# Performance work log

Measured on AMD Instinct MI355X. Metric: run time of the kernel, lower is better.

## Reference

```python
import jax, jax.numpy as jnp
import numpy as np

NEG_SLOPE = 0.2  # PyG GATv2Conv default negative_slope


def _gatv2(x, src, dst, Wl, Wr, att, bias, N, H, C):
    # GATv2: e_ij = att . leaky_relu(Wl x_j + Wr x_i); segment softmax over dst; scatter-add messages Wl x_j
    xl = (x @ Wl).reshape(N, H, C)  # source-side transform
    xr = (x @ Wr).reshape(N, H, C)  # target-side transform
    g = jax.nn.leaky_relu(xl[src] + xr[dst], NEG_SLOPE)  # [E, H, C]
    e = jnp.einsum('ehc,hc->eh', g, att)                 # [E, H]
    emax = jax.lax.stop_gradient(jax.ops.segment_max(e, dst, num_segments=N))
    p = jnp.exp(e - emax[dst])
    denom = jax.ops.segment_sum(p, dst, num_segments=N)
    alpha = p / denom[dst]                                # segment softmax [E, H]
    out = jax.ops.segment_sum(alpha[:, :, None] * xl[src], dst, num_segments=N)
    return out.reshape(N, H * C) + bias


def setup_inputs() -> dict:
    key = jax.random.key(0)
    N, E, F, H, C, L = 100000, 1000000, 128, 8, 10, 3
    ks = jax.random.split(key, 2 + 4 * L)
    inp = {
        'x': jax.random.normal(ks[0], (N, F), dtype=jnp.float32),
        'edge_index': jax.random.randint(ks[1], (2, E), 0, N, dtype=jnp.int32),
    }
    dims = [F] + [H * C] * (L - 1)
    for l in range(L):
        din = dims[l]
        s = 1.0 / np.sqrt(din)
        inp[f'Wl{l}'] = (jax.random.normal(ks[2 + 4 * l], (din, H * C)) * s).astype(jnp.float32)
        inp[f'Wr{l}'] = (jax.random.normal(ks[3 + 4 * l], (din, H * C)) * s).astype(jnp.float32)
        inp[f'att{l}'] = (jax.random.normal(ks[4 + 4 * l], (H, C)) * (1.0 / np.sqrt(C))).astype(jnp.float32)
        inp[f'b{l}'] = jnp.zeros((H * C,), jnp.float32)
    return inp


def reference(x, edge_index, Wl0, Wr0, att0, b0, Wl1, Wr1, att1, b1, Wl2, Wr2, att2, b2):
    N = x.shape[0]
    H, C = att0.shape
    # add self loops (PyG default add_self_loops=True)
    loops = jnp.arange(N, dtype=edge_index.dtype)
    src = jnp.concatenate([edge_index[0], loops])
    dst = jnp.concatenate([edge_index[1], loops])
    for Wl, Wr, att, b in ((Wl0, Wr0, att0, b0), (Wl1, Wr1, att1, b1), (Wl2, Wr2, att2, b2)):
        x = jax.nn.elu(_gatv2(x, src, dst, Wl, Wr, att, b, N, H, C))
    return x
```

## Files before the change

kernel.cpp:

```cpp
#include <hip/hip_runtime.h>
#include <cfloat>
#include <cmath>

#define HC 80
#define HH 8
#define CC 10

#define GAP(c) ((c) + ((((c) >> 5)) << 2))


__global__ void hist_kernel(const int* __restrict__ dst, int* __restrict__ counts, int E) {
    int i = blockIdx.x * blockDim.x + threadIdx.x;
    int stride = gridDim.x * blockDim.x;
    for (; i < E; i += stride) atomicAdd(&counts[dst[i]], 1);
}

__global__ void scan_kernel(const int* __restrict__ in, int* __restrict__ out, int n) {
    __shared__ int wsum[16];
    __shared__ int carry;
    if (threadIdx.x == 0) carry = 0;
    __syncthreads();
    int lane = threadIdx.x & 63, w = threadIdx.x >> 6;
    for (int base = 0; base < n; base += 1024) {
        int i = base + (int)threadIdx.x;
        int v = (i < n) ? in[i] : 0;
        int s = v;
        #pragma unroll
        for (int off = 1; off < 64; off <<= 1) {
            int t = __shfl_up(s, off, 64);
            if (lane >= off) s += t;
        }
        if (lane == 63) wsum[w] = s;
        __syncthreads();
        if (w == 0) {
            int ws = (lane < 16) ? wsum[lane] : 0;
            int ss = ws;
            #pragma unroll
            for (int off = 1; off < 16; off <<= 1) {
                int t = __shfl_up(ss, off, 64);
                if (lane >= off) ss += t;
            }
            if (lane < 16) wsum[lane] = ss - ws;
        }
        __syncthreads();
        int c = carry;
        if (i < n) out[i] = c + wsum[w] + s - v;
        __syncthreads();
        if (threadIdx.x == 1023) carry = c + wsum[15] + s;
    }
    __syncthreads();
    if (threadIdx.x == 0) out[n] = carry;
}

__global__ void scatter_kernel(const int* __restrict__ src, const int* __restrict__ dst,
                               int* __restrict__ cursor, int* __restrict__ csr, int E) {
    int i = blockIdx.x * blockDim.x + threadIdx.x;
    int stride = gridDim.x * blockDim.x;
    for (; i < E; i += stride) {
        int p = atomicAdd(&cursor[dst[i]], 1);
        csr[p] = src[i];
    }
}


__global__ __launch_bounds__(320) void gemm_big(
    const float* __restrict__ X, const float* __restrict__ Wl, const float* __restrict__ Wr,
    float* __restrict__ Yl, float* __restrict__ Yr, int N, int K)
{
    __shared__ float xs[16 * 140];
    __shared__ float ws[16 * 176];
    const int tid = threadIdx.x;
    const int rt = tid & 15;
    const int cg = tid >> 4;
    const int r0 = rt * 8;
    const int c0 = cg * 8;
    const int rG0 = GAP(r0);
    const int cG0 = GAP(c0);
    const int base = blockIdx.x * 128;

    float4 acc[8][2];
    #pragma unroll
    for (int i = 0; i < 8; ++i) {
        acc[i][0] = make_float4(0.f, 0.f, 0.f, 0.f);
        acc[i][1] = make_float4(0.f, 0.f, 0.f, 0.f);
    }

    for (int k0 = 0; k0 < K; k0 += 16) {
        __syncthreads();
        for (int idx = tid; idx < 512; idx += 320) {
            int r = idx >> 2, kc = (idx & 3) << 2;
            int n = base + r; if (n >= N) n = N - 1;
            float4 v = *(const float4*)(X + (size_t)n * K + k0 + kc);
            int rg = GAP(r);
            xs[(kc + 0) * 140 + rg] = v.x;
            xs[(kc + 1) * 140 + rg] = v.y;
            xs[(kc + 2) * 140 + rg] = v.z;
            xs[(kc + 3) * 140 + rg] = v.w;
        }
        {
            int r = rt;
            int c4 = cg * 4;
            float4 v = *(const float4*)(Wl + (size_t)(k0 + r) * HC + c4);
            *(float4*)&ws[r * 176 + GAP(c4)] = v;
            float4 u = *(const float4*)(Wr + (size_t)(k0 + r) * HC + c4);
            *(float4*)&ws[r * 176 + GAP(c4 + 80)] = u;
        }
        __syncthreads();

        #pragma unroll 4
        for (int k = 0; k < 16; ++k) {
            const float* xk = &xs[k * 140 + rG0];
            float4 xa = *(const float4*)(xk);
            float4 xb = *(const float4*)(xk + 4);
            const float* wk = &ws[k * 176 + cG0];
            float4 wa = *(const float4*)(wk);
            float4 wb = *(const float4*)(wk + 4);
            float xv[8] = {xa.x, xa.y, xa.z, xa.w, xb.x, xb.y, xb.z, xb.w};
            #pragma unroll
            for (int i = 0; i < 8; ++i) {
                acc[i][0].x += xv[i] * wa.x;
                acc[i][0].y += xv[i] * wa.y;
                acc[i][0].z += xv[i] * wa.z;
                acc[i][0].w += xv[i] * wa.w;
                acc[i][1].x += xv[i] * wb.x;
                acc[i][1].y += xv[i] * wb.y;
                acc[i][1].z += xv[i] * wb.z;
                acc[i][1].w += xv[i] * wb.w;
            }
        }
    }

    float* Ybase = (cg < 10) ? (Yl + c0) : (Yr + (c0 - 80));
    #pragma unroll
    for (int i = 0; i < 8; ++i) {
        int n = base + r0 + i;
        if (n < N) {
            float* yp = Ybase + (size_t)n * HC;
            *(float4*)yp = acc[i][0];
            *(float4*)(yp + 4) = acc[i][1];
        }
    }
}


__global__ __launch_bounds__(256) void aggregate_kernel(
    const float* __restrict__ xl, const float* __restrict__ xr,
    const int* __restrict__ csr, const int* __restrict__ offsets,
    const float* __restrict__ att, const float* __restrict__ bias,
    float* __restrict__ xout, int N) {
    const int tid = threadIdx.x;
    const int g = tid >> 3;
    const int h = tid & 7;
    const int n = blockIdx.x * 32 + g;
    if (n >= N) return;
    const float L2E = 1.4426950408889634f;

    float attv[10], xrv[10];
    #pragma unroll
    for (int j = 0; j < 5; ++j) {
        float2 a = *(const float2*)(att + h * CC + 2 * j);
        attv[2 * j] = a.x * L2E; attv[2 * j + 1] = a.y * L2E;
        float2 r = *(const float2*)(xr + (size_t)n * HC + h * CC + 2 * j);
        xrv[2 * j] = r.x; xrv[2 * j + 1] = r.y;
    }

    const int beg = offsets[n], end = offsets[n + 1];
    float m = -1e30f, s = 0.f;
    float acc[10];
    #pragma unroll
    for (int j = 0; j < 10; ++j) acc[j] = 0.f;

    int i = beg - 1;
    while (__any(i < end)) {
        if (i < end) {
            int src = (i < beg) ? n : csr[i];
            const float* xp = xl + (size_t)src * HC + h * CC;
            float xv[10];
            #pragma unroll
            for (int j = 0; j < 5; ++j) {
                float2 v = *(const float2*)(xp + 2 * j);
                xv[2 * j] = v.x; xv[2 * j + 1] = v.y;
            }
            float e = 0.f;
            #pragma unroll
            for (int j = 0; j < 10; ++j) {
                float t = xv[j] + xrv[j];
                float l = 0.6f * t + 0.4f * fabsf(t);
                e += l * attv[j];
            }
            float diff = e - m;
            if (__builtin_expect(diff > 8.0f, 0)) {
                float sc = exp2f(-diff);
                s = s * sc + 1.f;
                #pragma unroll
                for (int j = 0; j < 10; ++j) acc[j] = acc[j] * sc + xv[j];
                m = e;
            } else {
                float p = exp2f(diff);
                s += p;
                #pragma unroll
                for (int j = 0; j < 10; ++j) acc[j] += p * xv[j];
            }
        }
        ++i;
    }

    float inv = 1.f / s;
    float* op = xout + (size_t)n * HC + h * CC;
    #pragma unroll
    for (int j = 0; j < 5; ++j) {
        float2 b = *(const float2*)(bias + h * CC + 2 * j);
        float o0 = acc[2 * j] * inv + b.x;
        float o1 = acc[2 * j + 1] * inv + b.y;
        o0 = (o0 > 0.f) ? o0 : (__expf(o0) - 1.f);
        o1 = (o1 > 0.f) ? o1 : (__expf(o1) - 1.f);
        *(float2*)(op + 2 * j) = make_float2(o0, o1);
    }
}

extern "C" void kernel_launch(void* const* d_in, const int* in_sizes, int n_in,
                              void* d_out, int out_size, void* d_ws, size_t ws_size,
                              hipStream_t stream) {
    int N = out_size / HC;
    int E = in_sizes[1] / 2;
    int F = in_sizes[0] / N;

    const float* x   = (const float*)d_in[0];
    const int*   ei  = (const int*)d_in[1];
    const float* Wl[3]  = {(const float*)d_in[2], (const float*)d_in[6],  (const float*)d_in[10]};
    const float* Wr[3]  = {(const float*)d_in[3], (const float*)d_in[7],  (const float*)d_in[11]};
    const float* att[3] = {(const float*)d_in[4], (const float*)d_in[8],  (const float*)d_in[12]};
    const float* bb[3]  = {(const float*)d_in[5], (const float*)d_in[9],  (const float*)d_in[13]};

    size_t NF = (size_t)N * HC;
    float* xl = (float*)d_ws;
    float* xr = xl + NF;
    float* xb = xr + NF;
    int* counts  = (int*)(xb + NF);
    int* offsets = counts + (N + 1);
    int* cursor  = offsets + (N + 1);
    int* csr     = cursor + N;

    const int* srcv = ei;
    const int* dstv = ei + E;

    hipMemsetAsync(counts, 0, (size_t)(N + 1) * sizeof(int), stream);
    hist_kernel<<<1024, 256, 0, stream>>>(dstv, counts, E);
    scan_kernel<<<1, 1024, 0, stream>>>(counts, offsets, N);
    hipMemcpyAsync(cursor, offsets, (size_t)N * sizeof(int), hipMemcpyDeviceToDevice, stream);
    scatter_kernel<<<1024, 256, 0, stream>>>(srcv, dstv, cursor, csr, E);

    for (int l = 0; l < 3; ++l) {
        const float* xin = (l == 0) ? x : xb;
        int K = (l == 0) ? F : HC;
        gemm_big<<<(N + 127) / 128, 320, 0, stream>>>(xin, Wl[l], Wr[l], xl, xr, N, K);
        float* xout = (l == 2) ? (float*)d_out : xb;
        aggregate_kernel<<<(N + 31) / 32, 256, 0, stream>>>(xl, xr, csr, offsets, att[l], bb[l], xout, N);
    }
}
```

Before: 737.4 us.

## Double-buffer GEMM tiles and process aggregation nodes sorted by degree

```diff
diff --git a/kernel.cpp b/kernel.cpp
--- a/kernel.cpp
+++ b/kernel.cpp
@@ -63,12 +63,41 @@
 }
 
 
-__global__ __launch_bounds__(320) void gemm_big(
+__global__ void dhist_kernel(const int* __restrict__ counts, int* __restrict__ dhist, int N) {
+    int i = blockIdx.x * blockDim.x + threadIdx.x;
+    int st = gridDim.x * blockDim.x;
+    for (; i < N; i += st) atomicAdd(&dhist[min(counts[i], 63)], 1);
+}
+
+__global__ void dscan_kernel(const int* __restrict__ dhist, int* __restrict__ dcur) {
+    int lane = threadIdx.x;
+    int v = dhist[lane], s = v;
+    #pragma unroll
+    for (int off = 1; off < 64; off <<= 1) {
+        int t = __shfl_up(s, off, 64);
+        if (lane >= off) s += t;
+    }
+    dcur[lane] = s - v;
+}
+
+__global__ void dorder_kernel(const int* __restrict__ counts, int* __restrict__ dcur,
+                              int* __restrict__ order, int N) {
+    int i = blockIdx.x * blockDim.x + threadIdx.x;
+    int st = gridDim.x * blockDim.x;
+    for (; i < N; i += st) {
+        int b = min(counts[i], 63);
+        int p = atomicAdd(&dcur[b], 1);
+        order[p] = i;
+    }
+}
+
+
+__global__ __launch_bounds__(320, 4) void gemm_big(
     const float* __restrict__ X, const float* __restrict__ Wl, const float* __restrict__ Wr,
     float* __restrict__ Yl, float* __restrict__ Yr, int N, int K)
 {
-    __shared__ float xs[16 * 140];
-    __shared__ float ws[16 * 176];
+    __shared__ float xs[2][16 * 140];
+    __shared__ float ws[2][16 * 176];
     const int tid = threadIdx.x;
     const int rt = tid & 15;
     const int cg = tid >> 4;
@@ -78,6 +107,43 @@
     const int cG0 = GAP(c0);
     const int base = blockIdx.x * 128;
 
+    const int xr_0 = tid >> 2,         xk0 = (tid & 3) << 2;
+    const int xr_1 = (tid + 320) >> 2, xk1 = ((tid + 320) & 3) << 2;
+    const bool hasX1 = tid < 192;
+    const int wrow0 = tid / 40,      wc0 = tid % 40;
+    const int wrow1 = 8 + tid / 40,  wc1 = tid % 40;
+
+    float4 vx0, vx1, vw0, vw1;
+
+    auto loadTile = [&](int k0) {
+        int n0 = base + xr_0; if (n0 >= N) n0 = N - 1;
+        vx0 = *(const float4*)(X + (size_t)n0 * K + k0 + xk0);
+        if (hasX1) {
+            int n1 = base + xr_1; if (n1 >= N) n1 = N - 1;
+            vx1 = *(const float4*)(X + (size_t)n1 * K + k0 + xk1);
+        }
+        vw0 = (wc0 < 20) ? *(const float4*)(Wl + (size_t)(k0 + wrow0) * HC + wc0 * 4)
+                         : *(const float4*)(Wr + (size_t)(k0 + wrow0) * HC + (wc0 - 20) * 4);
+        vw1 = (wc1 < 20) ? *(const float4*)(Wl + (size_t)(k0 + wrow1) * HC + wc1 * 4)
+                         : *(const float4*)(Wr + (size_t)(k0 + wrow1) * HC + (wc1 - 20) * 4);
+    };
+    auto storeTile = [&](int b) {
+        int rg = GAP(xr_0);
+        xs[b][(xk0 + 0) * 140 + rg] = vx0.x;
+        xs[b][(xk0 + 1) * 140 + rg] = vx0.y;
+        xs[b][(xk0 + 2) * 140 + rg] = vx0.z;
+        xs[b][(xk0 + 3) * 140 + rg] = vx0.w;
+        if (hasX1) {
+            int rg1 = GAP(xr_1);
+            xs[b][(xk1 + 0) * 140 + rg1] = vx1.x;
+            xs[b][(xk1 + 1) * 140 + rg1] = vx1.y;
+            xs[b][(xk1 + 2) * 140 + rg1] = vx1.z;
+            xs[b][(xk1 + 3) * 140 + rg1] = vx1.w;
+        }
+        *(float4*)&ws[b][wrow0 * 176 + GAP(wc0 * 4)] = vw0;
+        *(float4*)&ws[b][wrow1 * 176 + GAP(wc1 * 4)] = vw1;
+    };
+
     float4 acc[8][2];
     #pragma unroll
     for (int i = 0; i < 8; ++i) {
@@ -85,34 +151,21 @@
         acc[i][1] = make_float4(0.f, 0.f, 0.f, 0.f);
     }
 
-    for (int k0 = 0; k0 < K; k0 += 16) {
-        __syncthreads();
-        for (int idx = tid; idx < 512; idx += 320) {
-            int r = idx >> 2, kc = (idx & 3) << 2;
-            int n = base + r; if (n >= N) n = N - 1;
-            float4 v = *(const float4*)(X + (size_t)n * K + k0 + kc);
-            int rg = GAP(r);
-            xs[(kc + 0) * 140 + rg] = v.x;
-            xs[(kc + 1) * 140 + rg] = v.y;
-            xs[(kc + 2) * 140 + rg] = v.z;
-            xs[(kc + 3) * 140 + rg] = v.w;
-        }
-        {
-            int r = rt;
-            int c4 = cg * 4;
-            float4 v = *(const float4*)(Wl + (size_t)(k0 + r) * HC + c4);
-            *(float4*)&ws[r * 176 + GAP(c4)] = v;
-            float4 u = *(const float4*)(Wr + (size_t)(k0 + r) * HC + c4);
-            *(float4*)&ws[r * 176 + GAP(c4 + 80)] = u;
-        }
-        __syncthreads();
+    loadTile(0);
+    storeTile(0);
+    __syncthreads();
+
+    const int nT = K >> 4;
+    for (int t = 0; t < nT; ++t) {
+        const int cur = t & 1;
+        if (t + 1 < nT) loadTile((t + 1) << 4);
 
         #pragma unroll 4
         for (int k = 0; k < 16; ++k) {
-            const float* xk = &xs[k * 140 + rG0];
+            const float* xk = &xs[cur][k * 140 + rG0];
             float4 xa = *(const float4*)(xk);
             float4 xb = *(const float4*)(xk + 4);
-            const float* wk = &ws[k * 176 + cG0];
+            const float* wk = &ws[cur][k * 176 + cG0];
             float4 wa = *(const float4*)(wk);
             float4 wb = *(const float4*)(wk + 4);
             float xv[8] = {xa.x, xa.y, xa.z, xa.w, xb.x, xb.y, xb.z, xb.w};
@@ -128,6 +181,9 @@
                 acc[i][1].w += xv[i] * wb.w;
             }
         }
+
+        if (t + 1 < nT) storeTile(cur ^ 1);
+        __syncthreads();
     }
 
     float* Ybase = (cg < 10) ? (Yl + c0) : (Yr + (c0 - 80));
@@ -146,13 +202,14 @@
 __global__ __launch_bounds__(256) void aggregate_kernel(
     const float* __restrict__ xl, const float* __restrict__ xr,
     const int* __restrict__ csr, const int* __restrict__ offsets,
+    const int* __restrict__ order,
     const float* __restrict__ att, const float* __restrict__ bias,
     float* __restrict__ xout, int N) {
     const int tid = threadIdx.x;
-    const int g = tid >> 3;
+    const int idx = blockIdx.x * 32 + (tid >> 3);
     const int h = tid & 7;
-    const int n = blockIdx.x * 32 + g;
-    if (n >= N) return;
+    if (idx >= N) return;
+    const int n = order[idx];
     const float L2E = 1.4426950408889634f;
 
     float attv[10], xrv[10];
@@ -240,21 +297,29 @@
     int* offsets = counts + (N + 1);
     int* cursor  = offsets + (N + 1);
     int* csr     = cursor + N;
+    int* dhist   = csr + E;
+    int* dcur    = dhist + 64;
+    int* order   = dcur + 64;
 
     const int* srcv = ei;
     const int* dstv = ei + E;
 
     hipMemsetAsync(counts, 0, (size_t)(N + 1) * sizeof(int), stream);
+    hipMemsetAsync(dhist, 0, 64 * sizeof(int), stream);
     hist_kernel<<<1024, 256, 0, stream>>>(dstv, counts, E);
     scan_kernel<<<1, 1024, 0, stream>>>(counts, offsets, N);
     hipMemcpyAsync(cursor, offsets, (size_t)N * sizeof(int), hipMemcpyDeviceToDevice, stream);
     scatter_kernel<<<1024, 256, 0, stream>>>(srcv, dstv, cursor, csr, E);
+    dhist_kernel<<<512, 256, 0, stream>>>(counts, dhist, N);
+    dscan_kernel<<<1, 64, 0, stream>>>(dhist, dcur);
+    dorder_kernel<<<512, 256, 0, stream>>>(counts, dcur, order, N);
 
     for (int l = 0; l < 3; ++l) {
         const float* xin = (l == 0) ? x : xb;
         int K = (l == 0) ? F : HC;
         gemm_big<<<(N + 127) / 128, 320, 0, stream>>>(xin, Wl[l], Wr[l], xl, xr, N, K);
         float* xout = (l == 2) ? (float*)d_out : xb;
-        aggregate_kernel<<<(N + 31) / 32, 256, 0, stream>>>(xl, xr, csr, offsets, att[l], bb[l], xout, N);
-    }
-}
+        aggregate_kernel<<<(N + 31) / 32, 256, 0, stream>>>(xl, xr, csr, offsets, order,
+                                                            att[l], bb[l], xout, N);
+    }
+}
```

After: 1.425 ms. 93.3% more time.

## Replace FP32 SIMT GEMM with split-bf16 MFMA GEMM

Applied to the files above, without the earlier changes.

```diff
diff --git a/kernel.cpp b/kernel.cpp
--- a/kernel.cpp
+++ b/kernel.cpp
@@ -6,7 +6,8 @@
 #define HH 8
 #define CC 10
 
-#define GAP(c) ((c) + ((((c) >> 5)) << 2))
+typedef __attribute__((ext_vector_type(8))) short bf16x8;
+typedef __attribute__((ext_vector_type(4))) float f32x4;
 
 
 __global__ void hist_kernel(const int* __restrict__ dst, int* __restrict__ counts, int E) {
@@ -63,81 +64,84 @@
 }
 
 
-__global__ __launch_bounds__(320) void gemm_big(
+__device__ __forceinline__ unsigned short f2bf(float x) {
+    unsigned u = __float_as_uint(x);
+    u += 0x7FFF + ((u >> 16) & 1);
+    return (unsigned short)(u >> 16);
+}
+
+__global__ __launch_bounds__(256, 4) void gemm_mfma(
     const float* __restrict__ X, const float* __restrict__ Wl, const float* __restrict__ Wr,
     float* __restrict__ Yl, float* __restrict__ Yr, int N, int K)
 {
-    __shared__ float xs[16 * 140];
-    __shared__ float ws[16 * 176];
+    __shared__ short wsb[2][160][40];
     const int tid = threadIdx.x;
-    const int rt = tid & 15;
-    const int cg = tid >> 4;
-    const int r0 = rt * 8;
-    const int c0 = cg * 8;
-    const int rG0 = GAP(r0);
-    const int cG0 = GAP(c0);
-    const int base = blockIdx.x * 128;
-
-    float4 acc[8][2];
-    #pragma unroll
-    for (int i = 0; i < 8; ++i) {
-        acc[i][0] = make_float4(0.f, 0.f, 0.f, 0.f);
-        acc[i][1] = make_float4(0.f, 0.f, 0.f, 0.f);
-    }
-
-    for (int k0 = 0; k0 < K; k0 += 16) {
-        __syncthreads();
-        for (int idx = tid; idx < 512; idx += 320) {
-            int r = idx >> 2, kc = (idx & 3) << 2;
-            int n = base + r; if (n >= N) n = N - 1;
-            float4 v = *(const float4*)(X + (size_t)n * K + k0 + kc);
-            int rg = GAP(r);
-            xs[(kc + 0) * 140 + rg] = v.x;
-            xs[(kc + 1) * 140 + rg] = v.y;
-            xs[(kc + 2) * 140 + rg] = v.z;
-            xs[(kc + 3) * 140 + rg] = v.w;
-        }
-        {
-            int r = rt;
-            int c4 = cg * 4;
-            float4 v = *(const float4*)(Wl + (size_t)(k0 + r) * HC + c4);
-            *(float4*)&ws[r * 176 + GAP(c4)] = v;
-            float4 u = *(const float4*)(Wr + (size_t)(k0 + r) * HC + c4);
-            *(float4*)&ws[r * 176 + GAP(c4 + 80)] = u;
-        }
-        __syncthreads();
-
-        #pragma unroll 4
-        for (int k = 0; k < 16; ++k) {
-            const float* xk = &xs[k * 140 + rG0];
-            float4 xa = *(const float4*)(xk);
-            float4 xb = *(const float4*)(xk + 4);
-            const float* wk = &ws[k * 176 + cG0];
-            float4 wa = *(const float4*)(wk);
-            float4 wb = *(const float4*)(wk + 4);
-            float xv[8] = {xa.x, xa.y, xa.z, xa.w, xb.x, xb.y, xb.z, xb.w};
-            #pragma unroll
-            for (int i = 0; i < 8; ++i) {
-                acc[i][0].x += xv[i] * wa.x;
-                acc[i][0].y += xv[i] * wa.y;
-                acc[i][0].z += xv[i] * wa.z;
-                acc[i][0].w += xv[i] * wa.w;
-                acc[i][1].x += xv[i] * wb.x;
-                acc[i][1].y += xv[i] * wb.y;
-                acc[i][1].z += xv[i] * wb.z;
-                acc[i][1].w += xv[i] * wb.w;
-            }
-        }
-    }
-
-    float* Ybase = (cg < 10) ? (Yl + c0) : (Yr + (c0 - 80));
-    #pragma unroll
-    for (int i = 0; i < 8; ++i) {
-        int n = base + r0 + i;
-        if (n < N) {
-            float* yp = Ybase + (size_t)n * HC;
-            *(float4*)yp = acc[i][0];
-            *(float4*)(yp + 4) = acc[i][1];
+    const int w = tid >> 6;
+    const int l = tid & 63;
+    const int lr = l & 15;
+    const int lg = l >> 4;
+    const int base = blockIdx.x * 64;
+
+    f32x4 acc[10];
+    #pragma unroll
+    for (int ct = 0; ct < 10; ++ct) acc[ct] = (f32x4){0.f, 0.f, 0.f, 0.f};
+
+    int arow = base + w * 16 + lr; if (arow >= N) arow = N - 1;
+    const int nch = (K + 31) >> 5;
+
+    for (int ch = 0; ch < nch; ++ch) {
+        const int k0 = ch << 5;
+        __syncthreads();
+        for (int e = tid; e < 5120; e += 256) {
+            int kr = e / 160, c = e - kr * 160;
+            int k = k0 + kr;
+            float x = 0.f;
+            if (k < K) x = (c < 80) ? Wl[k * 80 + c] : Wr[k * 80 + (c - 80)];
+            unsigned short h = f2bf(x);
+            wsb[0][c][kr] = (short)h;
+            wsb[1][c][kr] = (short)f2bf(x - __uint_as_float((unsigned)h << 16));
+        }
+        __syncthreads();
+
+        const int ks = k0 + lg * 8;
+        float xv[8];
+        if (ks < K) {
+            const float* xp = X + (size_t)arow * K + ks;
+            float4 t0 = *(const float4*)(xp);
+            float4 t1 = *(const float4*)(xp + 4);
+            xv[0] = t0.x; xv[1] = t0.y; xv[2] = t0.z; xv[3] = t0.w;
+            xv[4] = t1.x; xv[5] = t1.y; xv[6] = t1.z; xv[7] = t1.w;
+        } else {
+            #pragma unroll
+            for (int j = 0; j < 8; ++j) xv[j] = 0.f;
+        }
+        bf16x8 ah, al;
+        #pragma unroll
+        for (int j = 0; j < 8; ++j) {
+            unsigned short h = f2bf(xv[j]);
+            ah[j] = (short)h;
+            al[j] = (short)f2bf(xv[j] - __uint_as_float((unsigned)h << 16));
+        }
+
+        #pragma unroll
+        for (int ct = 0; ct < 10; ++ct) {
+            const int c = ct * 16 + lr;
+            bf16x8 bh = *(const bf16x8*)&wsb[0][c][lg * 8];
+            bf16x8 bl = *(const bf16x8*)&wsb[1][c][lg * 8];
+            acc[ct] = __builtin_amdgcn_mfma_f32_16x16x32_bf16(ah, bh, acc[ct], 0, 0, 0);
+            acc[ct] = __builtin_amdgcn_mfma_f32_16x16x32_bf16(al, bh, acc[ct], 0, 0, 0);
+            acc[ct] = __builtin_amdgcn_mfma_f32_16x16x32_bf16(ah, bl, acc[ct], 0, 0, 0);
+        }
+    }
+
+    #pragma unroll
+    for (int ct = 0; ct < 10; ++ct) {
+        const int c = ct * 16 + lr;
+        float* Yb = (c < 80) ? (Yl + c) : (Yr + (c - 80));
+        #pragma unroll
+        for (int j = 0; j < 4; ++j) {
+            int r = base + w * 16 + lg * 4 + j;
+            if (r < N) Yb[(size_t)r * HC] = acc[ct][j];
         }
     }
 }
@@ -149,9 +153,8 @@
     const float* __restrict__ att, const float* __restrict__ bias,
     float* __restrict__ xout, int N) {
     const int tid = threadIdx.x;
-    const int g = tid >> 3;
+    const int n = blockIdx.x * 32 + (tid >> 3);
     const int h = tid & 7;
-    const int n = blockIdx.x * 32 + g;
     if (n >= N) return;
     const float L2E = 1.4426950408889634f;
 
@@ -185,8 +188,8 @@
             #pragma unroll
             for (int j = 0; j < 10; ++j) {
                 float t = xv[j] + xrv[j];
-                float l = 0.6f * t + 0.4f * fabsf(t);
-                e += l * attv[j];
+                float lk = 0.6f * t + 0.4f * fabsf(t);
+                e += lk * attv[j];
             }
             float diff = e - m;
             if (__builtin_expect(diff > 8.0f, 0)) {
@@ -253,8 +256,9 @@
     for (int l = 0; l < 3; ++l) {
         const float* xin = (l == 0) ? x : xb;
         int K = (l == 0) ? F : HC;
-        gemm_big<<<(N + 127) / 128, 320, 0, stream>>>(xin, Wl[l], Wr[l], xl, xr, N, K);
+        gemm_mfma<<<(N + 63) / 64, 256, 0, stream>>>(xin, Wl[l], Wr[l], xl, xr, N, K);
         float* xout = (l == 2) ? (float*)d_out : xb;
-        aggregate_kernel<<<(N + 31) / 32, 256, 0, stream>>>(xl, xr, csr, offsets, att[l], bb[l], xout, N);
-    }
-}
+        aggregate_kernel<<<(N + 31) / 32, 256, 0, stream>>>(xl, xr, csr, offsets,
+                                                            att[l], bb[l], xout, N);
+    }
+}
```

New measurement: 713.8 us. -3.2%, faster.
